# Kernel optimization log

Hardware: AMD Instinct MI355X
Metric: run time of the kernel (lower is better)

The kernel has to match this reference:

```python
import jax, jax.numpy as jnp
import numpy as np

N_NODES = 100000
N_EDGES = 1600000
IN_DIM, HID_DIM, OUT_DIM = 128, 64, 128


def _glorot(key, shape):
    fan_in, fan_out = shape[1], shape[0]
    lim = jnp.sqrt(6.0 / (fan_in + fan_out)).astype(jnp.float32)
    return jax.random.uniform(key, shape, jnp.float32, -lim, lim)


def setup_inputs() -> dict:
    key = jax.random.key(0)
    ks = jax.random.split(key, 8)
    x = jax.random.normal(ks[0], (N_NODES, IN_DIM), jnp.float32)
    edge_index = jax.random.randint(ks[1], (2, N_EDGES), 0, N_NODES, jnp.int32)
    # SAGEConv params: lin_l (applied to aggregated neighbors, has bias),
    # lin_r (applied to root/self, no bias) -- PyG convention.
    W_l1 = _glorot(ks[2], (HID_DIM, IN_DIM))
    W_r1 = _glorot(ks[3], (HID_DIM, IN_DIM))
    b1 = jnp.zeros((HID_DIM,), jnp.float32)
    W_l2 = _glorot(ks[4], (OUT_DIM, HID_DIM))
    W_r2 = _glorot(ks[5], (OUT_DIM, HID_DIM))
    b2 = jnp.zeros((OUT_DIM,), jnp.float32)
    return {"x": x, "edge_index": edge_index,
            "W_l1": W_l1, "W_r1": W_r1, "b1": b1,
            "W_l2": W_l2, "W_r2": W_r2, "b2": b2}


def _mean_aggregate(x, src, dst, num_nodes):
    # gather source features per edge, scatter-sum at destination, divide by in-degree
    msg = x[src]                                             # [E, d]
    summed = jax.ops.segment_sum(msg, dst, num_segments=num_nodes)   # [N, d]
    deg = jax.ops.segment_sum(jnp.ones_like(dst, jnp.float32), dst,
                              num_segments=num_nodes)        # [N]
    return summed / jnp.maximum(deg, 1.0)[:, None]


def _sage_conv(x, src, dst, W_l, W_r, b, num_nodes):
    aggr = _mean_aggregate(x, src, dst, num_nodes)
    # out = lin_l(mean_j x_j) + lin_r(x_i)
    return aggr @ W_l.T + b + x @ W_r.T


def reference(x, edge_index, W_l1, W_r1, b1, W_l2, W_r2, b2):
    src, dst = edge_index[0], edge_index[1]
    n = x.shape[0]
    h = _sage_conv(x, src, dst, W_l1, W_r1, b1, n)
    h = jax.nn.relu(h)  # dropout is identity in eval mode
    out = _sage_conv(h, src, dst, W_l2, W_r2, b2, n)
    return out
```

## Files before the change

kernel.cpp:

```cpp
#include <hip/hip_runtime.h>

#define TPB 256
#define BK_SH 8
#define NBMAX 512
#define TILE 4096
#define CAP 8192
#define CAPR 16384
#define M2LD 72

typedef unsigned short ushort_t;
typedef unsigned int uint_t;
typedef __attribute__((ext_vector_type(8))) __bf16 bf8v;
typedef __attribute__((ext_vector_type(4))) float f4v;

__device__ inline ushort_t f2bf(float f) {
    uint_t u = __float_as_uint(f);
    return (ushort_t)((u + 0x7FFFu + ((u >> 16) & 1u)) >> 16);
}
__device__ inline uint_t pack2(float a, float b) {
    return (uint_t)f2bf(a) | ((uint_t)f2bf(b) << 16);
}

union u4bf8 {
    uint4 u;
    bf8v b;
};

__device__ inline void addrow(float* acc, uint4 v) {
    acc[0] += __uint_as_float(v.x << 16);
    acc[1] += __uint_as_float(v.x & 0xFFFF0000u);
    acc[2] += __uint_as_float(v.y << 16);
    acc[3] += __uint_as_float(v.y & 0xFFFF0000u);
    acc[4] += __uint_as_float(v.z << 16);
    acc[5] += __uint_as_float(v.z & 0xFFFF0000u);
    acc[6] += __uint_as_float(v.w << 16);
    acc[7] += __uint_as_float(v.w & 0xFFFF0000u);
}

__global__ __launch_bounds__(TPB) void cvt_w_kernel(const float* __restrict__ Wl1,
                                                    const float* __restrict__ Wr1,
                                                    const float* __restrict__ Wl2,
                                                    const float* __restrict__ Wr2,
                                                    ushort_t* __restrict__ wl1b,
                                                    ushort_t* __restrict__ wr1b,
                                                    ushort_t* __restrict__ wcat,
                                                    int* __restrict__ bcursor) {
    int i = blockIdx.x * TPB + threadIdx.x;
    if (i < NBMAX) bcursor[i] = i * CAPR;
    if (i < 8192) {
        wl1b[i] = f2bf(Wl1[i]);
        wr1b[i] = f2bf(Wr1[i]);
    }
    if (i < 16384) {
        int c = i >> 7, k = i & 127;
        wcat[i] = (k < 64) ? f2bf(Wl2[c * 64 + k]) : f2bf(Wr2[c * 64 + (k - 64)]);
    }
}

struct ScatterSmem {
    uint_t rec[TILE];
    ushort_t bb[TILE];
    int hist[NBMAX];
    int start[NBMAX];
    int cur[NBMAX];
    int gbase[NBMAX];
    int ss[TPB];
};

__global__ __launch_bounds__(TPB) void fat_kernel(
    const int* __restrict__ src, const int* __restrict__ dst,
    int* __restrict__ bcursor, uint_t* __restrict__ recs, int E, int NB, int SB,
    const float* __restrict__ xf, const ushort_t* __restrict__ Wl,
    const ushort_t* __restrict__ Wr, ushort_t* __restrict__ y1b,
    float* __restrict__ zf, int n) {
    __shared__ ScatterSmem sm;
    const int tid = threadIdx.x;
    if ((int)blockIdx.x < SB) {
        const int t0 = blockIdx.x * TILE;
        const int cnt = min(TILE, E - t0);
        for (int i = tid; i < NBMAX; i += TPB) sm.hist[i] = 0;
        __syncthreads();

        int myS[16], myD[16];
#pragma unroll
        for (int j = 0; j < 16; ++j) {
            int e = t0 + j * TPB + tid;
            if (e < E) {
                myS[j] = src[e];
                myD[j] = dst[e];
                atomicAdd(&sm.hist[myD[j] >> BK_SH], 1);
            } else {
                myD[j] = -1;
            }
        }
        __syncthreads();

        int h0 = sm.hist[2 * tid], h1 = sm.hist[2 * tid + 1];
        int sum2 = h0 + h1;
        sm.ss[tid] = sum2;
        __syncthreads();
        for (int off = 1; off < TPB; off <<= 1) {
            int a = (tid >= off) ? sm.ss[tid - off] : 0;
            __syncthreads();
            sm.ss[tid] += a;
            __syncthreads();
        }
        int ex = sm.ss[tid] - sum2;
        sm.start[2 * tid] = ex;
        sm.start[2 * tid + 1] = ex + h0;
        sm.cur[2 * tid] = ex;
        sm.cur[2 * tid + 1] = ex + h0;
        __syncthreads();

#pragma unroll
        for (int j = 0; j < 16; ++j) {
            if (myD[j] >= 0) {
                int b = myD[j] >> BK_SH;
                int p = atomicAdd(&sm.cur[b], 1);
                sm.rec[p] = ((uint_t)myS[j] << BK_SH) | (uint_t)(myD[j] & ((1 << BK_SH) - 1));
                sm.bb[p] = (ushort_t)b;
            }
        }
        __syncthreads();

        for (int b = tid; b < NB; b += TPB) {
            int c = sm.hist[b];
            sm.gbase[b] = c ? atomicAdd(&bcursor[b], c) : 0;
        }
        __syncthreads();

        for (int i = tid; i < cnt; i += TPB) {
            int b = sm.bb[i];
            recs[sm.gbase[b] + (i - sm.start[b])] = sm.rec[i];
        }
    } else {
        const int wave = tid >> 6;
        const int lane = tid & 63;
        const int l16 = lane & 15;
        const int quad = lane >> 4;
        const int node0 = ((int)blockIdx.x - SB) * 128 + wave * 32;
        const int koff = quad * 8;

        bf8v wl[4][4], wr[4][4];
#pragma unroll
        for (int ct = 0; ct < 4; ++ct)
#pragma unroll
            for (int kt = 0; kt < 4; ++kt) {
                wl[ct][kt] = *(const bf8v*)(Wl + (ct * 16 + l16) * 128 + kt * 32 + koff);
                wr[ct][kt] = *(const bf8v*)(Wr + (ct * 16 + l16) * 128 + kt * 32 + koff);
            }

        f4v accY[2][4], accZ[2][4];
#pragma unroll
        for (int mt = 0; mt < 2; ++mt)
#pragma unroll
            for (int ct = 0; ct < 4; ++ct) {
                accY[mt][ct] = (f4v)(0.0f);
                accZ[mt][ct] = (f4v)(0.0f);
            }

#pragma unroll
        for (int mt = 0; mt < 2; ++mt) {
            int row = node0 + mt * 16 + l16;
            row = min(row, n - 1);
            bf8v a[4];
#pragma unroll
            for (int kt = 0; kt < 4; ++kt) {
                const float* p = xf + (long long)row * 128 + kt * 32 + koff;
                float4 f0 = *(const float4*)(p);
                float4 f1 = *(const float4*)(p + 4);
                u4bf8 cvt;
                cvt.u.x = pack2(f0.x, f0.y);
                cvt.u.y = pack2(f0.z, f0.w);
                cvt.u.z = pack2(f1.x, f1.y);
                cvt.u.w = pack2(f1.z, f1.w);
                a[kt] = cvt.b;
            }
#pragma unroll
            for (int ct = 0; ct < 4; ++ct)
#pragma unroll
                for (int kt = 0; kt < 4; ++kt) {
                    accY[mt][ct] = __builtin_amdgcn_mfma_f32_16x16x32_bf16(
                        a[kt], wl[ct][kt], accY[mt][ct], 0, 0, 0);
                    accZ[mt][ct] = __builtin_amdgcn_mfma_f32_16x16x32_bf16(
                        a[kt], wr[ct][kt], accZ[mt][ct], 0, 0, 0);
                }
        }

#pragma unroll
        for (int ct = 0; ct < 4; ++ct) {
            const int col = ct * 16 + l16;
#pragma unroll
            for (int mt = 0; mt < 2; ++mt) {
                int rbase = node0 + mt * 16 + quad * 4;
#pragma unroll
                for (int r = 0; r < 4; ++r) {
                    int g = rbase + r;
                    if (g >= n) continue;
                    y1b[(long long)g * 64 + col] = f2bf(accY[mt][ct][r]);
                    zf[(long long)g * 64 + col] = accZ[mt][ct][r];
                }
            }
        }
    }
}

__global__ __launch_bounds__(TPB) void bucket_build_kernel(const uint_t* __restrict__ recs,
                                                           const int* __restrict__ bcursor,
                                                           int* __restrict__ rs_beg,
                                                           int* __restrict__ rs_end,
                                                           int* __restrict__ perm, int n) {
    __shared__ int nh[TPB];
    __shared__ int ncur[TPB];
    __shared__ int sscan[TPB];
    __shared__ uint_t stage[CAP];
    const int b = blockIdx.x;
    const int tid = threadIdx.x;
    const int gb = b * CAPR;
    const int cnt = bcursor[b] - gb;
    nh[tid] = 0;
    __syncthreads();
    for (int i = tid; i < cnt; i += TPB)
        atomicAdd(&nh[recs[gb + i] & 255], 1);
    __syncthreads();
    int v = nh[tid];
    sscan[tid] = v;
    __syncthreads();
    for (int off = 1; off < TPB; off <<= 1) {
        int a = (tid >= off) ? sscan[tid - off] : 0;
        __syncthreads();
        sscan[tid] += a;
        __syncthreads();
    }
    int ex = sscan[tid] - v;
    int g = (b << BK_SH) + tid;
    if (g < n) {
        rs_beg[g] = gb + ex;
        rs_end[g] = gb + ex + v;
    }
    ncur[tid] = ex;
    __syncthreads();
    if (cnt <= CAP) {
        for (int i = tid; i < cnt; i += TPB) {
            uint_t r = recs[gb + i];
            int p = atomicAdd(&ncur[r & 255], 1);
            stage[p] = r >> BK_SH;
        }
        __syncthreads();
        for (int i = tid; i < cnt; i += TPB)
            perm[gb + i] = (int)stage[i];
    } else {
        for (int i = tid; i < cnt; i += TPB) {
            uint_t r = recs[gb + i];
            int p = atomicAdd(&ncur[r & 255], 1);
            perm[gb + p] = (int)(r >> BK_SH);
        }
    }
}

__global__ __launch_bounds__(TPB) void csr_mean8_kernel(
    const ushort_t* __restrict__ feat, const int* __restrict__ rs_beg,
    const int* __restrict__ rs_end, const int* __restrict__ perm,
    const float* __restrict__ zf, const float* __restrict__ bias,
    ushort_t* __restrict__ outb, int n) {
    long long gt = (long long)blockIdx.x * TPB + threadIdx.x;
    int w = (int)(gt >> 3);
    if (w >= n) return;
    const int cl = threadIdx.x & 7;
    const int beg = rs_beg[w], end = rs_end[w];
    float acc[8];
#pragma unroll
    for (int j = 0; j < 8; ++j) acc[j] = 0.0f;
    const uint4* fp = (const uint4*)feat;
    int e = beg;
    for (; e + 8 <= end; e += 8) {
        int s[8];
#pragma unroll
        for (int j = 0; j < 8; ++j) s[j] = perm[e + j];
        uint4 v[8];
#pragma unroll
        for (int j = 0; j < 8; ++j) v[j] = fp[((long long)s[j] << 3) + cl];
#pragma unroll
        for (int j = 0; j < 8; ++j) addrow(acc, v[j]);
    }
    for (; e + 4 <= end; e += 4) {
        int s0 = perm[e], s1 = perm[e + 1], s2 = perm[e + 2], s3 = perm[e + 3];
        uint4 v0 = fp[((long long)s0 << 3) + cl];
        uint4 v1 = fp[((long long)s1 << 3) + cl];
        uint4 v2 = fp[((long long)s2 << 3) + cl];
        uint4 v3 = fp[((long long)s3 << 3) + cl];
        addrow(acc, v0);
        addrow(acc, v1);
        addrow(acc, v2);
        addrow(acc, v3);
    }
    for (; e < end; ++e) {
        int s = perm[e];
        uint4 v = fp[((long long)s << 3) + cl];
        addrow(acc, v);
    }
    float d = (float)(end - beg);
    float inv = d > 0.f ? 1.f / d : 0.f;
    float r[8];
#pragma unroll
    for (int j = 0; j < 8; ++j) r[j] = acc[j] * inv;
    const float* zp = zf + (long long)w * 64 + cl * 8;
    float4 z0 = *(const float4*)(zp);
    float4 z1 = *(const float4*)(zp + 4);
    const float* bp = bias + cl * 8;
    float4 b0 = *(const float4*)(bp);
    float4 b1v = *(const float4*)(bp + 4);
    r[0] = fmaxf(r[0] + z0.x + b0.x, 0.0f);
    r[1] = fmaxf(r[1] + z0.y + b0.y, 0.0f);
    r[2] = fmaxf(r[2] + z0.z + b0.z, 0.0f);
    r[3] = fmaxf(r[3] + z0.w + b0.w, 0.0f);
    r[4] = fmaxf(r[4] + z1.x + b1v.x, 0.0f);
    r[5] = fmaxf(r[5] + z1.y + b1v.y, 0.0f);
    r[6] = fmaxf(r[6] + z1.z + b1v.z, 0.0f);
    r[7] = fmaxf(r[7] + z1.w + b1v.w, 0.0f);
    uint4 o4;
    o4.x = pack2(r[0], r[1]);
    o4.y = pack2(r[2], r[3]);
    o4.z = pack2(r[4], r[5]);
    o4.w = pack2(r[6], r[7]);
    ((uint4*)(outb + (long long)w * 64))[cl] = o4;
}

__global__ __launch_bounds__(TPB) void out_fused_kernel(
    const ushort_t* __restrict__ hb, const int* __restrict__ rs_beg,
    const int* __restrict__ rs_end, const int* __restrict__ perm,
    const ushort_t* __restrict__ Wc, const float* __restrict__ b2,
    float* __restrict__ out, int n) {
    __shared__ ushort_t m2[64 * M2LD];
    const int tid = threadIdx.x;
    const int node0 = blockIdx.x * 64;
    const int oct = tid >> 3;
    const int cl = tid & 7;
    const uint4* fp = (const uint4*)hb;

#pragma unroll
    for (int half = 0; half < 2; ++half) {
        int widx = oct + half * 32;
        int w = node0 + widx;
        float acc[8];
#pragma unroll
        for (int j = 0; j < 8; ++j) acc[j] = 0.0f;
        float inv = 0.0f;
        if (w < n) {
            const int beg = rs_beg[w], end = rs_end[w];
            int e = beg;
            for (; e + 8 <= end; e += 8) {
                int s[8];
#pragma unroll
                for (int j = 0; j < 8; ++j) s[j] = perm[e + j];
                uint4 v[8];
#pragma unroll
                for (int j = 0; j < 8; ++j) v[j] = fp[((long long)s[j] << 3) + cl];
#pragma unroll
                for (int j = 0; j < 8; ++j) addrow(acc, v[j]);
            }
            for (; e + 4 <= end; e += 4) {
                int s0 = perm[e], s1 = perm[e + 1], s2 = perm[e + 2], s3 = perm[e + 3];
                uint4 v0 = fp[((long long)s0 << 3) + cl];
                uint4 v1 = fp[((long long)s1 << 3) + cl];
                uint4 v2 = fp[((long long)s2 << 3) + cl];
                uint4 v3 = fp[((long long)s3 << 3) + cl];
                addrow(acc, v0);
                addrow(acc, v1);
                addrow(acc, v2);
                addrow(acc, v3);
            }
            for (; e < end; ++e) {
                int s = perm[e];
                uint4 v = fp[((long long)s << 3) + cl];
                addrow(acc, v);
            }
            float d = (float)(end - beg);
            inv = d > 0.f ? 1.f / d : 0.f;
        }
        uint4 o4;
        o4.x = pack2(acc[0] * inv, acc[1] * inv);
        o4.y = pack2(acc[2] * inv, acc[3] * inv);
        o4.z = pack2(acc[4] * inv, acc[5] * inv);
        o4.w = pack2(acc[6] * inv, acc[7] * inv);
        *(uint4*)(m2 + widx * M2LD + cl * 8) = o4;
    }
    __syncthreads();

    const int wave = tid >> 6;
    const int lane = tid & 63;
    const int l16 = lane & 15;
    const int quad = lane >> 4;
    const int cb = wave * 32;
    const int koff = quad * 8;

    bf8v wb[2][4];
#pragma unroll
    for (int ct = 0; ct < 2; ++ct)
#pragma unroll
        for (int kt = 0; kt < 4; ++kt)
            wb[ct][kt] = *(const bf8v*)(Wc + (cb + ct * 16 + l16) * 128 + kt * 32 + koff);

    f4v acc2[4][2];
#pragma unroll
    for (int mt = 0; mt < 4; ++mt)
#pragma unroll
        for (int ct = 0; ct < 2; ++ct) acc2[mt][ct] = (f4v)(0.0f);

#pragma unroll
    for (int mt = 0; mt < 4; ++mt) {
        int rl = mt * 16 + l16;
        int row = min(node0 + rl, n - 1);
        bf8v a[4];
        a[0] = *(const bf8v*)(m2 + rl * M2LD + koff);
        a[1] = *(const bf8v*)(m2 + rl * M2LD + 32 + koff);
        a[2] = *(const bf8v*)(hb + (long long)row * 64 + koff);
        a[3] = *(const bf8v*)(hb + (long long)row * 64 + 32 + koff);
#pragma unroll
        for (int ct = 0; ct < 2; ++ct)
#pragma unroll
            for (int kt = 0; kt < 4; ++kt)
                acc2[mt][ct] = __builtin_amdgcn_mfma_f32_16x16x32_bf16(
                    a[kt], wb[ct][kt], acc2[mt][ct], 0, 0, 0);
    }

#pragma unroll
    for (int ct = 0; ct < 2; ++ct) {
        const int col = cb + ct * 16 + l16;
        const float bv = b2[col];
#pragma unroll
        for (int mt = 0; mt < 4; ++mt) {
            int rbase = node0 + mt * 16 + quad * 4;
#pragma unroll
            for (int r = 0; r < 4; ++r) {
                int g = rbase + r;
                if (g >= n) continue;
                __builtin_nontemporal_store(acc2[mt][ct][r] + bv,
                                            &out[(long long)g * 128 + col]);
            }
        }
    }
}

extern "C" void kernel_launch(void* const* d_in, const int* in_sizes, int n_in,
                              void* d_out, int out_size, void* d_ws, size_t ws_size,
                              hipStream_t stream) {
    const float* x = (const float*)d_in[0];
    const int* ei = (const int*)d_in[1];
    const float* Wl1 = (const float*)d_in[2];
    const float* Wr1 = (const float*)d_in[3];
    const float* b1 = (const float*)d_in[4];
    const float* Wl2 = (const float*)d_in[5];
    const float* Wr2 = (const float*)d_in[6];
    const float* b2 = (const float*)d_in[7];
    float* out = (float*)d_out;

    const int n = in_sizes[0] / 128;
    const int E = in_sizes[1] / 2;
    const int* src = ei;
    const int* dst = ei + E;
    const int NB = (n + 255) >> BK_SH;

    char* wsb = (char*)d_ws;
    auto A = [](size_t v) { return (v + 63) & ~(size_t)63; };
    int* bcursor = (int*)wsb;                      size_t o = NBMAX;
    int* rs_beg = (int*)wsb + o;                   o += A(n);
    int* rs_end = (int*)wsb + o;                   o += A(n);
    uint_t* recs = (uint_t*)((int*)wsb + o);       o += (size_t)NB * CAPR;
    int* perm = (int*)wsb + o;                     o += (size_t)NB * CAPR;
    ushort_t* wl1b = (ushort_t*)((int*)wsb + o);   o += 4096;
    ushort_t* wr1b = (ushort_t*)((int*)wsb + o);   o += 4096;
    ushort_t* wcat = (ushort_t*)((int*)wsb + o);   o += 8192;
    ushort_t* fb = (ushort_t*)((int*)wsb + o);     o += A((size_t)n * 32);
    ushort_t* hbuf = (ushort_t*)((int*)wsb + o);   o += A((size_t)n * 32);
    float* zf = (float*)wsb + o;

    cvt_w_kernel<<<64, TPB, 0, stream>>>(Wl1, Wr1, Wl2, Wr2, wl1b, wr1b, wcat, bcursor);

    const int SB = (E + TILE - 1) / TILE;
    const int LB = (n + 127) / 128;
    fat_kernel<<<SB + LB, TPB, 0, stream>>>(src, dst, bcursor, recs, E, NB, SB,
                                            x, wl1b, wr1b, fb, zf, n);

    bucket_build_kernel<<<NB, TPB, 0, stream>>>(recs, bcursor, rs_beg, rs_end, perm, n);

    const int mblocks = (int)(((long long)n * 8 + TPB - 1) / TPB);
    const int oblocks = (n + 63) / 64;

    csr_mean8_kernel<<<mblocks, TPB, 0, stream>>>(fb, rs_beg, rs_end, perm, zf, b1, hbuf, n);
    out_fused_kernel<<<oblocks, TPB, 0, stream>>>(hbuf, rs_beg, rs_end, perm, wcat, b2, out, n);
}
```

Before: 240.6 us.

## Drop weight-conversion kernel, convert weights inline, widen output kernel to 512 threads

Removes the separate kernel that converted the weights to bf16 and initialised the bucket cursors. The consumers now load fp32 weights and convert them in registers, and the cursor is zeroed with a memset, with the bucket offset added at use. The output kernel moves to 512 threads: each thread aggregates one node instead of two, and each wave computes 16 output columns instead of 32. This cuts one launch and raises parallelism in the final kernel, at the cost of every block redoing the weight conversion and of a memset node.

```diff
diff --git a/kernel.cpp b/kernel.cpp
--- a/kernel.cpp
+++ b/kernel.cpp
@@ -1,6 +1,7 @@
 #include <hip/hip_runtime.h>
 
 #define TPB 256
+#define TPO 512
 #define BK_SH 8
 #define NBMAX 512
 #define TILE 4096
@@ -25,6 +26,17 @@
     uint4 u;
     bf8v b;
 };
+
+__device__ inline bf8v ldcvt8(const float* p) {
+    float4 f0 = *(const float4*)(p);
+    float4 f1 = *(const float4*)(p + 4);
+    u4bf8 cvt;
+    cvt.u.x = pack2(f0.x, f0.y);
+    cvt.u.y = pack2(f0.z, f0.w);
+    cvt.u.z = pack2(f1.x, f1.y);
+    cvt.u.w = pack2(f1.z, f1.w);
+    return cvt.b;
+}
 
 __device__ inline void addrow(float* acc, uint4 v) {
     acc[0] += __uint_as_float(v.x << 16);
@@ -37,26 +49,6 @@
     acc[7] += __uint_as_float(v.w & 0xFFFF0000u);
 }
 
-__global__ __launch_bounds__(TPB) void cvt_w_kernel(const float* __restrict__ Wl1,
-                                                    const float* __restrict__ Wr1,
-                                                    const float* __restrict__ Wl2,
-                                                    const float* __restrict__ Wr2,
-                                                    ushort_t* __restrict__ wl1b,
-                                                    ushort_t* __restrict__ wr1b,
-                                                    ushort_t* __restrict__ wcat,
-                                                    int* __restrict__ bcursor) {
-    int i = blockIdx.x * TPB + threadIdx.x;
-    if (i < NBMAX) bcursor[i] = i * CAPR;
-    if (i < 8192) {
-        wl1b[i] = f2bf(Wl1[i]);
-        wr1b[i] = f2bf(Wr1[i]);
-    }
-    if (i < 16384) {
-        int c = i >> 7, k = i & 127;
-        wcat[i] = (k < 64) ? f2bf(Wl2[c * 64 + k]) : f2bf(Wr2[c * 64 + (k - 64)]);
-    }
-}
-
 struct ScatterSmem {
     uint_t rec[TILE];
     ushort_t bb[TILE];
@@ -70,8 +62,8 @@
 __global__ __launch_bounds__(TPB) void fat_kernel(
     const int* __restrict__ src, const int* __restrict__ dst,
     int* __restrict__ bcursor, uint_t* __restrict__ recs, int E, int NB, int SB,
-    const float* __restrict__ xf, const ushort_t* __restrict__ Wl,
-    const ushort_t* __restrict__ Wr, ushort_t* __restrict__ y1b,
+    const float* __restrict__ xf, const float* __restrict__ Wl1,
+    const float* __restrict__ Wr1, ushort_t* __restrict__ y1b,
     float* __restrict__ zf, int n) {
     __shared__ ScatterSmem sm;
     const int tid = threadIdx.x;
@@ -125,7 +117,7 @@
 
         for (int b = tid; b < NB; b += TPB) {
             int c = sm.hist[b];
-            sm.gbase[b] = c ? atomicAdd(&bcursor[b], c) : 0;
+            sm.gbase[b] = c ? (b * CAPR + atomicAdd(&bcursor[b], c)) : 0;
         }
         __syncthreads();
 
@@ -146,8 +138,9 @@
         for (int ct = 0; ct < 4; ++ct)
 #pragma unroll
             for (int kt = 0; kt < 4; ++kt) {
-                wl[ct][kt] = *(const bf8v*)(Wl + (ct * 16 + l16) * 128 + kt * 32 + koff);
-                wr[ct][kt] = *(const bf8v*)(Wr + (ct * 16 + l16) * 128 + kt * 32 + koff);
+                int c = ct * 16 + l16;
+                wl[ct][kt] = ldcvt8(Wl1 + c * 128 + kt * 32 + koff);
+                wr[ct][kt] = ldcvt8(Wr1 + c * 128 + kt * 32 + koff);
             }
 
         f4v accY[2][4], accZ[2][4];
@@ -165,17 +158,8 @@
             row = min(row, n - 1);
             bf8v a[4];
 #pragma unroll
-            for (int kt = 0; kt < 4; ++kt) {
-                const float* p = xf + (long long)row * 128 + kt * 32 + koff;
-                float4 f0 = *(const float4*)(p);
-                float4 f1 = *(const float4*)(p + 4);
-                u4bf8 cvt;
-                cvt.u.x = pack2(f0.x, f0.y);
-                cvt.u.y = pack2(f0.z, f0.w);
-                cvt.u.z = pack2(f1.x, f1.y);
-                cvt.u.w = pack2(f1.z, f1.w);
-                a[kt] = cvt.b;
-            }
+            for (int kt = 0; kt < 4; ++kt)
+                a[kt] = ldcvt8(xf + (long long)row * 128 + kt * 32 + koff);
 #pragma unroll
             for (int ct = 0; ct < 4; ++ct)
 #pragma unroll
@@ -217,7 +201,7 @@
     const int b = blockIdx.x;
     const int tid = threadIdx.x;
     const int gb = b * CAPR;
-    const int cnt = bcursor[b] - gb;
+    const int cnt = bcursor[b];
     nh[tid] = 0;
     __syncthreads();
     for (int i = tid; i < cnt; i += TPB)
@@ -326,11 +310,11 @@
     ((uint4*)(outb + (long long)w * 64))[cl] = o4;
 }
 
-__global__ __launch_bounds__(TPB) void out_fused_kernel(
+__global__ __launch_bounds__(TPO) void out_fused_kernel(
     const ushort_t* __restrict__ hb, const int* __restrict__ rs_beg,
     const int* __restrict__ rs_end, const int* __restrict__ perm,
-    const ushort_t* __restrict__ Wc, const float* __restrict__ b2,
-    float* __restrict__ out, int n) {
+    const float* __restrict__ Wl2, const float* __restrict__ Wr2,
+    const float* __restrict__ b2, float* __restrict__ out, int n) {
     __shared__ ushort_t m2[64 * M2LD];
     const int tid = threadIdx.x;
     const int node0 = blockIdx.x * 64;
@@ -338,10 +322,8 @@
     const int cl = tid & 7;
     const uint4* fp = (const uint4*)hb;
 
-#pragma unroll
-    for (int half = 0; half < 2; ++half) {
-        int widx = oct + half * 32;
-        int w = node0 + widx;
+    {
+        int w = node0 + oct;
         float acc[8];
 #pragma unroll
         for (int j = 0; j < 8; ++j) acc[j] = 0.0f;
@@ -383,7 +365,7 @@
         o4.y = pack2(acc[2] * inv, acc[3] * inv);
         o4.z = pack2(acc[4] * inv, acc[5] * inv);
         o4.w = pack2(acc[6] * inv, acc[7] * inv);
-        *(uint4*)(m2 + widx * M2LD + cl * 8) = o4;
+        *(uint4*)(m2 + oct * M2LD + cl * 8) = o4;
     }
     __syncthreads();
 
@@ -391,21 +373,21 @@
     const int lane = tid & 63;
     const int l16 = lane & 15;
     const int quad = lane >> 4;
-    const int cb = wave * 32;
+    const int cb = wave * 16;
     const int koff = quad * 8;
 
-    bf8v wb[2][4];
-#pragma unroll
-    for (int ct = 0; ct < 2; ++ct)
-#pragma unroll
-        for (int kt = 0; kt < 4; ++kt)
-            wb[ct][kt] = *(const bf8v*)(Wc + (cb + ct * 16 + l16) * 128 + kt * 32 + koff);
-
-    f4v acc2[4][2];
-#pragma unroll
-    for (int mt = 0; mt < 4; ++mt)
-#pragma unroll
-        for (int ct = 0; ct < 2; ++ct) acc2[mt][ct] = (f4v)(0.0f);
+    bf8v wb[4];
+    {
+        int c = cb + l16;
+        wb[0] = ldcvt8(Wl2 + c * 64 + koff);
+        wb[1] = ldcvt8(Wl2 + c * 64 + 32 + koff);
+        wb[2] = ldcvt8(Wr2 + c * 64 + koff);
+        wb[3] = ldcvt8(Wr2 + c * 64 + 32 + koff);
+    }
+
+    f4v acc2[4];
+#pragma unroll
+    for (int mt = 0; mt < 4; ++mt) acc2[mt] = (f4v)(0.0f);
 
 #pragma unroll
     for (int mt = 0; mt < 4; ++mt) {
@@ -417,16 +399,13 @@
         a[2] = *(const bf8v*)(hb + (long long)row * 64 + koff);
         a[3] = *(const bf8v*)(hb + (long long)row * 64 + 32 + koff);
 #pragma unroll
-        for (int ct = 0; ct < 2; ++ct)
-#pragma unroll
-            for (int kt = 0; kt < 4; ++kt)
-                acc2[mt][ct] = __builtin_amdgcn_mfma_f32_16x16x32_bf16(
-                    a[kt], wb[ct][kt], acc2[mt][ct], 0, 0, 0);
-    }
-
-#pragma unroll
-    for (int ct = 0; ct < 2; ++ct) {
-        const int col = cb + ct * 16 + l16;
+        for (int kt = 0; kt < 4; ++kt)
+            acc2[mt] = __builtin_amdgcn_mfma_f32_16x16x32_bf16(
+                a[kt], wb[kt], acc2[mt], 0, 0, 0);
+    }
+
+    {
+        const int col = cb + l16;
         const float bv = b2[col];
 #pragma unroll
         for (int mt = 0; mt < 4; ++mt) {
@@ -435,7 +414,7 @@
             for (int r = 0; r < 4; ++r) {
                 int g = rbase + r;
                 if (g >= n) continue;
-                __builtin_nontemporal_store(acc2[mt][ct][r] + bv,
+                __builtin_nontemporal_store(acc2[mt][r] + bv,
                                             &out[(long long)g * 128 + col]);
             }
         }
@@ -468,19 +447,16 @@
     int* rs_end = (int*)wsb + o;                   o += A(n);
     uint_t* recs = (uint_t*)((int*)wsb + o);       o += (size_t)NB * CAPR;
     int* perm = (int*)wsb + o;                     o += (size_t)NB * CAPR;
-    ushort_t* wl1b = (ushort_t*)((int*)wsb + o);   o += 4096;
-    ushort_t* wr1b = (ushort_t*)((int*)wsb + o);   o += 4096;
-    ushort_t* wcat = (ushort_t*)((int*)wsb + o);   o += 8192;
     ushort_t* fb = (ushort_t*)((int*)wsb + o);     o += A((size_t)n * 32);
     ushort_t* hbuf = (ushort_t*)((int*)wsb + o);   o += A((size_t)n * 32);
     float* zf = (float*)wsb + o;
 
-    cvt_w_kernel<<<64, TPB, 0, stream>>>(Wl1, Wr1, Wl2, Wr2, wl1b, wr1b, wcat, bcursor);
+    hipMemsetAsync(bcursor, 0, NBMAX * sizeof(int), stream);
 
     const int SB = (E + TILE - 1) / TILE;
     const int LB = (n + 127) / 128;
     fat_kernel<<<SB + LB, TPB, 0, stream>>>(src, dst, bcursor, recs, E, NB, SB,
-                                            x, wl1b, wr1b, fb, zf, n);
+                                            x, Wl1, Wr1, fb, zf, n);
 
     bucket_build_kernel<<<NB, TPB, 0, stream>>>(recs, bcursor, rs_beg, rs_end, perm, n);
 
@@ -488,5 +464,6 @@
     const int oblocks = (n + 63) / 64;
 
     csr_mean8_kernel<<<mblocks, TPB, 0, stream>>>(fb, rs_beg, rs_end, perm, zf, b1, hbuf, n);
-    out_fused_kernel<<<oblocks, TPB, 0, stream>>>(hbuf, rs_beg, rs_end, perm, wcat, b2, out, n);
-}
+    out_fused_kernel<<<oblocks, TPO, 0, stream>>>(hbuf, rs_beg, rs_end, perm,
+                                                  Wl2, Wr2, b2, out, n);
+}
```

After: 259.3 us. 7.8% more time.
